# Optimization experiments

Measured on AMD Instinct MI355X. Metric: run time of the kernel, lower is better.

Reference implementation:

```python
import jax, jax.numpy as jnp
import numpy as np

EMBED_DIM = 2048
NUM_HEADS = 32
NUM_KV_HEADS = 8
HEAD_DIM = EMBED_DIM // NUM_HEADS          # 64
GROUP = NUM_HEADS // NUM_KV_HEADS          # 4 queries per KV head
BATCH, SEQ = 2, 2048


def setup_inputs() -> dict:
    key = jax.random.key(0)
    ks = jax.random.split(key, 9)
    s_in = 1.0 / np.sqrt(EMBED_DIM)
    kv_dim = NUM_KV_HEADS * HEAD_DIM
    return {
        "x":      jax.random.normal(ks[0], (BATCH, SEQ, EMBED_DIM), jnp.float32),
        "Wq":     jax.random.normal(ks[1], (EMBED_DIM, EMBED_DIM), jnp.float32) * s_in,
        "bq":     jnp.zeros((EMBED_DIM,), jnp.float32),
        "Wk":     jax.random.normal(ks[2], (EMBED_DIM, kv_dim), jnp.float32) * s_in,
        "bk":     jnp.zeros((kv_dim,), jnp.float32),
        "Wv":     jax.random.normal(ks[3], (EMBED_DIM, kv_dim), jnp.float32) * s_in,
        "bv":     jnp.zeros((kv_dim,), jnp.float32),
        "Wo":     jax.random.normal(ks[4], (EMBED_DIM, EMBED_DIM), jnp.float32) * s_in,
        "bo":     jnp.zeros((EMBED_DIM,), jnp.float32),
    }


def reference(x, Wq, bq, Wk, bk, Wv, bv, Wo, bo):
    B, S, _ = x.shape
    # Projections (torch Linear == x @ W + b with W stored as [in, out] here)
    q = (x @ Wq + bq).reshape(B, S, NUM_KV_HEADS, GROUP, HEAD_DIM)  # grouped heads
    k = (x @ Wk + bk).reshape(B, S, NUM_KV_HEADS, HEAD_DIM)
    v = (x @ Wv + bv).reshape(B, S, NUM_KV_HEADS, HEAD_DIM)

    scale = 1.0 / np.sqrt(HEAD_DIM)
    # scores[b, h, g, s, t] = q[b, s, h, g, :] . k[b, t, h, :]
    # (repeat_interleave of K across the group dim == broadcasting over g)
    scores = jnp.einsum("bshgd,bthd->bhgst", q, k) * scale
    attn = jax.nn.softmax(scores, axis=-1)
    out = jnp.einsum("bhgst,bthd->bshgd", attn, v)  # [B, S, kvh, g, D]
    out = out.reshape(B, S, EMBED_DIM)
    return out @ Wo + bo
```

## Files before the change

### kernel.cpp

```cpp
#include <hip/hip_runtime.h>


typedef __attribute__((ext_vector_type(8)))  short bf16x8;
typedef __attribute__((ext_vector_type(4)))  float f32x4;
typedef __attribute__((ext_vector_type(16))) float f32x16;

#define DEVI static __device__ __forceinline__

DEVI short f2b(float f){
  unsigned u = __builtin_bit_cast(unsigned, f);
  u += 0x7FFFu + ((u >> 16) & 1u);
  return (short)(u >> 16);
}
DEVI float b2f(short s){
  unsigned u = ((unsigned)(unsigned short)s) << 16;
  return __builtin_bit_cast(float, u);
}
DEVI unsigned pack2(float a, float b){
  unsigned ua = __builtin_bit_cast(unsigned, a) + 0x8000u;
  unsigned ub = __builtin_bit_cast(unsigned, b) + 0x8000u;
  return __builtin_amdgcn_perm(ub, ua, 0x07060302u);
}

typedef __attribute__((address_space(3))) unsigned       lds_u32;
typedef __attribute__((address_space(1))) const unsigned gbl_u32;
DEVI void glds16(const short* g, short* l){
  __builtin_amdgcn_global_load_lds((gbl_u32*)g, (lds_u32*)l, 16, 0, 0);
}

__global__ void cast_kernel(const float* __restrict__ in, short* __restrict__ out, int n){
  int i = (blockIdx.x * 256 + threadIdx.x) * 8;
  if(i >= n) return;
  float4 a = *(const float4*)(in + i);
  float4 b = *(const float4*)(in + i + 4);
  bf16x8 v;
  v[0]=f2b(a.x); v[1]=f2b(a.y); v[2]=f2b(a.z); v[3]=f2b(a.w);
  v[4]=f2b(b.x); v[5]=f2b(b.y); v[6]=f2b(b.z); v[7]=f2b(b.w);
  *(bf16x8*)(out + i) = v;
}

__global__ void prep_kernel(const float* __restrict__ Wq, const float* __restrict__ Wk,
                            const float* __restrict__ Wv, const float* __restrict__ Wo,
                            const float* __restrict__ bq, const float* __restrict__ bk,
                            const float* __restrict__ bv,
                            short* __restrict__ WT, short* __restrict__ WoT,
                            float* __restrict__ bqkv){
  __shared__ __align__(16) short tile[64*72];
  const int gy = blockIdx.y;
  const int t = threadIdx.x;
  if(gy >= 80){
    int i = blockIdx.x * 256 + t;
    if(i < 3072) bqkv[i] = (i < 2048) ? bq[i] : (i < 2560 ? bk[i-2048] : bv[i-2560]);
    return;
  }
  const float* src; short* dst; int ldin, by;
  if(gy < 32)      { src = Wq; dst = WT;             ldin = 2048; by = gy;    }
  else if(gy < 40) { src = Wk; dst = WT + 2048*2048; ldin =  512; by = gy-32; }
  else if(gy < 48) { src = Wv; dst = WT + 2560*2048; ldin =  512; by = gy-40; }
  else             { src = Wo; dst = WoT;            ldin = 2048; by = gy-48; }
  const int tr = blockIdx.x * 64;
  const int tc = by * 64;
  for(int c = t; c < 512; c += 256){
    int r = c >> 3, g = c & 7;
    const float* p = src + (size_t)(tr + r) * ldin + tc + g*8;
    bf16x8 v;
    #pragma unroll
    for(int e = 0; e < 8; e++) v[e] = f2b(p[e]);
    *(bf16x8*)&tile[r*72 + g*8] = v;
  }
  __syncthreads();
  for(int c = t; c < 512; c += 256){
    int r = c >> 3, g = c & 7;
    bf16x8 v;
    #pragma unroll
    for(int e = 0; e < 8; e++) v[e] = tile[(g*8+e)*72 + r];
    *(bf16x8*)(dst + (size_t)(tc + r) * 2048 + tr + g*8) = v;
  }
}

__global__ void transpose_bf16_kernel(const short* __restrict__ in, short* __restrict__ out,
                                      int ldin, int ldout){
  __shared__ __align__(16) short tile[64*72];
  const int tr = blockIdx.x * 64;
  const int tc = blockIdx.y * 64;
  const int t = threadIdx.x;
  for(int c = t; c < 512; c += 256){
    int r = c >> 3, g = c & 7;
    *(bf16x8*)&tile[r*72 + g*8] = *(const bf16x8*)(in + (size_t)(tr + r) * ldin + tc + g*8);
  }
  __syncthreads();
  for(int c = t; c < 512; c += 256){
    int r = c >> 3, g = c & 7;
    bf16x8 v;
    #pragma unroll
    for(int e = 0; e < 8; e++) v[e] = tile[(g*8+e)*72 + r];
    *(bf16x8*)(out + (size_t)(tc + r) * ldout + tr + g*8) = v;
  }
}

template<bool OUT_F32>
__global__ __launch_bounds__(256, 2)
void gemm_bt_kernel(const short* __restrict__ A, const short* __restrict__ BT,
                    const float* __restrict__ bias, void* __restrict__ C,
                    int M, int N, int K, int scale_cols, float qscale){
  __shared__ __align__(16) short As[128*32];
  __shared__ __align__(16) short Bs[128*32];
  const int m0 = blockIdx.x * 128;
  const int n0 = blockIdx.y * 128;
  const int tid = threadIdx.x;
  const int wave = tid >> 6, lane = tid & 63;
  const int l16 = lane & 15, quad = lane >> 4;
  const int wm = (wave >> 1) * 64, wn = (wave & 1) * 64;

  const short* gA = A  + (size_t)(m0 + wave*32 + (lane>>2))*K + (lane&3)*8;
  const short* gB = BT + (size_t)(n0 + wave*32 + (lane>>2))*K + (lane&3)*8;
  short* lA = As + wave*32*32;
  short* lB = Bs + wave*32*32;

  f32x4 acc[4][4];
  #pragma unroll
  for(int i=0;i<4;i++)
    #pragma unroll
    for(int j=0;j<4;j++) acc[i][j] = (f32x4)(0.0f);

  for(int k0 = 0; k0 < K; k0 += 32){
    glds16(gA + k0,                lA);
    glds16(gA + 16*(size_t)K + k0, lA + 512);
    glds16(gB + k0,                lB);
    glds16(gB + 16*(size_t)K + k0, lB + 512);
    __syncthreads();
    bf16x8 af[4], bfr[4];
    #pragma unroll
    for(int i=0;i<4;i++){
      af[i]  = *(const bf16x8*)&As[(wm + i*16 + l16)*32 + quad*8];
      bfr[i] = *(const bf16x8*)&Bs[(wn + i*16 + l16)*32 + quad*8];
    }
    #pragma unroll
    for(int i=0;i<4;i++)
      #pragma unroll
      for(int j=0;j<4;j++)
        acc[i][j] = __builtin_amdgcn_mfma_f32_16x16x32_bf16(af[i], bfr[j], acc[i][j], 0, 0, 0);
    __syncthreads();
  }

  #pragma unroll
  for(int j=0;j<4;j++){
    int col = n0 + wn + j*16 + l16;
    float bb = bias[col];
    float sc = (col < scale_cols) ? qscale : 1.0f;
    #pragma unroll
    for(int i=0;i<4;i++){
      #pragma unroll
      for(int r=0;r<4;r++){
        size_t row = (size_t)(m0 + wm + i*16 + quad*4 + r);
        float v = (acc[i][j][r] + bb) * sc;
        if(OUT_F32) ((float*)C)[row*(size_t)N + col] = v;
        else        ((short*)C)[row*(size_t)N + col] = f2b(v);
      }
    }
  }
}

__global__ __launch_bounds__(256, 4)
void attn_kernel(const short* __restrict__ Qg, const short* __restrict__ Kg,
                 const short* __restrict__ VT, short* __restrict__ Og, int ldq){
  const int qt  = blockIdx.x;
  const int kvh = blockIdx.y;
  const int b   = blockIdx.z;
  const int tid = threadIdx.x;
  const int wave = tid >> 6, lane = tid & 63;
  const int c = lane & 31, h = lane >> 5;
  const int head = kvh*4 + wave;
  const int q0 = qt * 32;

  __shared__ __align__(16) short Ks[64*72];
  __shared__ __align__(16) short Vs[64*72];
  __shared__ __align__(16) short Ps[4][32*72];
  __shared__ __align__(16) float lS[4][32];

  bf16x8 qreg[4];
  #pragma unroll
  for(int ks=0; ks<4; ks++)
    qreg[ks] = *(const bf16x8*)(Qg + (size_t)(b*2048 + q0 + c)*ldq + head*64 + ks*16 + h*8);

  float lsum = 0.0f;
  f32x16 oacc[2];
  oacc[0] = (f32x16)(0.0f);
  oacc[1] = (f32x16)(0.0f);

  const short* gK = Kg + (size_t)(b*2048 + (tid>>3))*ldq + kvh*64 + (tid&7)*8;
  const short* gV = VT + (size_t)(kvh*64 + (tid>>3))*4096 + b*2048 + (tid&7)*8;
  short* sK = &Ks[(tid>>3)*72 + (tid&7)*8];
  short* sV = &Vs[(tid>>3)*72 + (tid&7)*8];
  const size_t kHalf = (size_t)32 * ldq;

  bf16x8 kr0 = *(const bf16x8*)(gK);
  bf16x8 kr1 = *(const bf16x8*)(gK + kHalf);
  bf16x8 vr0 = *(const bf16x8*)(gV);
  bf16x8 vr1 = *(const bf16x8*)(gV + 32*4096);

  for(int t0 = 0; t0 < 2048; t0 += 64){
    if(t0) __syncthreads();
    *(bf16x8*)sK            = kr0;
    *(bf16x8*)(sK + 32*72)  = kr1;
    *(bf16x8*)sV            = vr0;
    *(bf16x8*)(sV + 32*72)  = vr1;
    __syncthreads();
    if(t0 + 64 < 2048){
      const short* nK = gK + (size_t)(t0 + 64)*ldq;
      const short* nV = gV + (t0 + 64);
      kr0 = *(const bf16x8*)(nK);
      kr1 = *(const bf16x8*)(nK + kHalf);
      vr0 = *(const bf16x8*)(nV);
      vr1 = *(const bf16x8*)(nV + 32*4096);
    }

    f32x16 st[2];
    st[0] = (f32x16)(0.0f);
    st[1] = (f32x16)(0.0f);
    #pragma unroll
    for(int ks=0; ks<4; ks++){
      #pragma unroll
      for(int kb=0; kb<2; kb++){
        bf16x8 ak = *(const bf16x8*)&Ks[(kb*32 + c)*72 + ks*16 + h*8];
        st[kb] = __builtin_amdgcn_mfma_f32_32x32x16_bf16(ak, qreg[ks], st[kb], 0, 0, 0);
      }
    }

    float sum = 0.0f;
    #pragma unroll
    for(int kb=0; kb<2; kb++){
      #pragma unroll
      for(int g2=0; g2<4; g2++){
        float p0 = exp2f(st[kb][g2*4+0]);
        float p1 = exp2f(st[kb][g2*4+1]);
        float p2 = exp2f(st[kb][g2*4+2]);
        float p3 = exp2f(st[kb][g2*4+3]);
        sum += (p0 + p1) + (p2 + p3);
        uint2 w; w.x = pack2(p0, p1); w.y = pack2(p2, p3);
        *(uint2*)&Ps[wave][c*72 + kb*32 + g2*8 + 4*h] = w;
      }
    }
    lsum += sum;

    #pragma unroll
    for(int ks=0; ks<4; ks++){
      bf16x8 ap = *(const bf16x8*)&Ps[wave][c*72 + ks*16 + h*8];
      #pragma unroll
      for(int nb=0; nb<2; nb++){
        bf16x8 av = *(const bf16x8*)&Vs[(nb*32 + c)*72 + ks*16 + h*8];
        oacc[nb] = __builtin_amdgcn_mfma_f32_32x32x16_bf16(ap, av, oacc[nb], 0, 0, 0);
      }
    }
  }

  lsum += __shfl_xor(lsum, 32);
  if(h == 0) lS[wave][c] = lsum;
  f32x4 l4[4];
  #pragma unroll
  for(int g2=0; g2<4; g2++){
    f32x4 t = *(const f32x4*)&lS[wave][8*g2 + 4*h];
    l4[g2][0]=1.0f/t[0]; l4[g2][1]=1.0f/t[1]; l4[g2][2]=1.0f/t[2]; l4[g2][3]=1.0f/t[3];
  }
  #pragma unroll
  for(int nb=0; nb<2; nb++){
    int col = head*64 + nb*32 + c;
    #pragma unroll
    for(int e=0; e<16; e++){
      int row = q0 + (e&3) + 8*(e>>2) + 4*h;
      Og[(size_t)(b*2048 + row)*2048 + col] = f2b(oacc[nb][e] * l4[e>>2][e&3]);
    }
  }
}

extern "C" void kernel_launch(void* const* d_in, const int* in_sizes, int n_in,
                              void* d_out, int out_size, void* d_ws, size_t ws_size,
                              hipStream_t stream){
  const float* x  = (const float*)d_in[0];
  const float* Wq = (const float*)d_in[1];
  const float* bq = (const float*)d_in[2];
  const float* Wk = (const float*)d_in[3];
  const float* bk = (const float*)d_in[4];
  const float* Wv = (const float*)d_in[5];
  const float* bv = (const float*)d_in[6];
  const float* Wo = (const float*)d_in[7];
  const float* bo = (const float*)d_in[8];

  char* ws = (char*)d_ws;
  short* WT   = (short*)(ws);
  short* WoT  = (short*)(ws + 25165824);
  short* xb   = (short*)(ws + 33554432);
  short* QKV  = (short*)(ws + 50331648);
  short* VTb  = (short*)(ws + 75497472);
  float* bqkv = (float*)(ws + 79691776);
  short* AO   = xb;

  cast_kernel<<<4096, 256, 0, stream>>>(x, xb, 8388608);
  prep_kernel<<<dim3(32,81), 256, 0, stream>>>(Wq, Wk, Wv, Wo, bq, bk, bv, WT, WoT, bqkv);

  gemm_bt_kernel<false><<<dim3(32,24), 256, 0, stream>>>(xb, WT, bqkv, QKV,
                                                         4096, 3072, 2048,
                                                         2048, 0.1803368801111244f);

  transpose_bf16_kernel<<<dim3(64,8), 256, 0, stream>>>(QKV + 2560, VTb, 3072, 4096);

  attn_kernel<<<dim3(64,8,2), 256, 0, stream>>>(QKV, QKV + 2048, VTb, AO, 3072);

  gemm_bt_kernel<true><<<dim3(32,16), 256, 0, stream>>>(AO, WoT, bo, (float*)d_out,
                                                        4096, 2048, 2048, 0, 1.0f);
}
```

Measured before the change: 346.5 us.

## Process 64 queries per attention block to reuse K/V tiles across two query groups

Each wave of the attention kernel now handles two 32-row query groups against each staged K/V tile, doubling the query tile to 64 and halving the grid. This halves global K/V loads and LDS staging per query and gives each wave more independent MFMAs to interleave. The exponential switches to the hardware exp2 builtin. The costs are more accumulator registers (launch bounds lowered to 2 blocks per SM), a larger LDS P buffer, and only 1024 blocks, which may reduce occupancy and latency hiding.

```diff
diff --git a/kernel.cpp b/kernel.cpp
--- a/kernel.cpp
+++ b/kernel.cpp
@@ -6,15 +6,17 @@
 typedef __attribute__((ext_vector_type(16))) float f32x16;
 
 #define DEVI static __device__ __forceinline__
+
+#if __has_builtin(__builtin_amdgcn_exp2f)
+#define EXP2F __builtin_amdgcn_exp2f
+#else
+#define EXP2F exp2f
+#endif
 
 DEVI short f2b(float f){
   unsigned u = __builtin_bit_cast(unsigned, f);
   u += 0x7FFFu + ((u >> 16) & 1u);
   return (short)(u >> 16);
-}
-DEVI float b2f(short s){
-  unsigned u = ((unsigned)(unsigned short)s) << 16;
-  return __builtin_bit_cast(float, u);
 }
 DEVI unsigned pack2(float a, float b){
   unsigned ua = __builtin_bit_cast(unsigned, a) + 0x8000u;
@@ -161,7 +163,7 @@
   }
 }
 
-__global__ __launch_bounds__(256, 4)
+__global__ __launch_bounds__(256, 2)
 void attn_kernel(const short* __restrict__ Qg, const short* __restrict__ Kg,
                  const short* __restrict__ VT, short* __restrict__ Og, int ldq){
   const int qt  = blockIdx.x;
@@ -171,22 +173,27 @@
   const int wave = tid >> 6, lane = tid & 63;
   const int c = lane & 31, h = lane >> 5;
   const int head = kvh*4 + wave;
-  const int q0 = qt * 32;
+  const int q0 = qt * 64;
 
   __shared__ __align__(16) short Ks[64*72];
   __shared__ __align__(16) short Vs[64*72];
-  __shared__ __align__(16) short Ps[4][32*72];
-  __shared__ __align__(16) float lS[4][32];
-
-  bf16x8 qreg[4];
+  __shared__ __align__(16) short Ps[4][64*72];
+  __shared__ __align__(16) float lS[4][2][32];
+
+  bf16x8 qreg[4][2];
   #pragma unroll
   for(int ks=0; ks<4; ks++)
-    qreg[ks] = *(const bf16x8*)(Qg + (size_t)(b*2048 + q0 + c)*ldq + head*64 + ks*16 + h*8);
-
-  float lsum = 0.0f;
-  f32x16 oacc[2];
-  oacc[0] = (f32x16)(0.0f);
-  oacc[1] = (f32x16)(0.0f);
+    #pragma unroll
+    for(int qg=0; qg<2; qg++)
+      qreg[ks][qg] = *(const bf16x8*)(Qg + (size_t)(b*2048 + q0 + qg*32 + c)*ldq
+                                         + head*64 + ks*16 + h*8);
+
+  float lsum[2] = {0.0f, 0.0f};
+  f32x16 oacc[2][2];
+  #pragma unroll
+  for(int qg=0; qg<2; qg++)
+    #pragma unroll
+    for(int nb=0; nb<2; nb++) oacc[qg][nb] = (f32x16)(0.0f);
 
   const short* gK = Kg + (size_t)(b*2048 + (tid>>3))*ldq + kvh*64 + (tid&7)*8;
   const short* gV = VT + (size_t)(kvh*64 + (tid>>3))*4096 + b*2048 + (tid&7)*8;
@@ -215,60 +222,73 @@
       vr1 = *(const bf16x8*)(nV + 32*4096);
     }
 
-    f32x16 st[2];
-    st[0] = (f32x16)(0.0f);
-    st[1] = (f32x16)(0.0f);
+    f32x16 st[2][2];
+    st[0][0] = (f32x16)(0.0f); st[0][1] = (f32x16)(0.0f);
+    st[1][0] = (f32x16)(0.0f); st[1][1] = (f32x16)(0.0f);
     #pragma unroll
     for(int ks=0; ks<4; ks++){
       #pragma unroll
       for(int kb=0; kb<2; kb++){
         bf16x8 ak = *(const bf16x8*)&Ks[(kb*32 + c)*72 + ks*16 + h*8];
-        st[kb] = __builtin_amdgcn_mfma_f32_32x32x16_bf16(ak, qreg[ks], st[kb], 0, 0, 0);
-      }
-    }
-
-    float sum = 0.0f;
-    #pragma unroll
-    for(int kb=0; kb<2; kb++){
-      #pragma unroll
-      for(int g2=0; g2<4; g2++){
-        float p0 = exp2f(st[kb][g2*4+0]);
-        float p1 = exp2f(st[kb][g2*4+1]);
-        float p2 = exp2f(st[kb][g2*4+2]);
-        float p3 = exp2f(st[kb][g2*4+3]);
-        sum += (p0 + p1) + (p2 + p3);
-        uint2 w; w.x = pack2(p0, p1); w.y = pack2(p2, p3);
-        *(uint2*)&Ps[wave][c*72 + kb*32 + g2*8 + 4*h] = w;
-      }
-    }
-    lsum += sum;
+        st[kb][0] = __builtin_amdgcn_mfma_f32_32x32x16_bf16(ak, qreg[ks][0], st[kb][0], 0, 0, 0);
+        st[kb][1] = __builtin_amdgcn_mfma_f32_32x32x16_bf16(ak, qreg[ks][1], st[kb][1], 0, 0, 0);
+      }
+    }
+
+    #pragma unroll
+    for(int qg=0; qg<2; qg++){
+      float sum = 0.0f;
+      #pragma unroll
+      for(int kb=0; kb<2; kb++){
+        #pragma unroll
+        for(int g2=0; g2<4; g2++){
+          float p0 = EXP2F(st[kb][qg][g2*4+0]);
+          float p1 = EXP2F(st[kb][qg][g2*4+1]);
+          float p2 = EXP2F(st[kb][qg][g2*4+2]);
+          float p3 = EXP2F(st[kb][qg][g2*4+3]);
+          sum += (p0 + p1) + (p2 + p3);
+          uint2 w; w.x = pack2(p0, p1); w.y = pack2(p2, p3);
+          *(uint2*)&Ps[wave][(qg*32 + c)*72 + kb*32 + g2*8 + 4*h] = w;
+        }
+      }
+      lsum[qg] += sum;
+    }
 
     #pragma unroll
     for(int ks=0; ks<4; ks++){
-      bf16x8 ap = *(const bf16x8*)&Ps[wave][c*72 + ks*16 + h*8];
+      bf16x8 ap0 = *(const bf16x8*)&Ps[wave][(c     )*72 + ks*16 + h*8];
+      bf16x8 ap1 = *(const bf16x8*)&Ps[wave][(32 + c)*72 + ks*16 + h*8];
       #pragma unroll
       for(int nb=0; nb<2; nb++){
         bf16x8 av = *(const bf16x8*)&Vs[(nb*32 + c)*72 + ks*16 + h*8];
-        oacc[nb] = __builtin_amdgcn_mfma_f32_32x32x16_bf16(ap, av, oacc[nb], 0, 0, 0);
-      }
-    }
-  }
-
-  lsum += __shfl_xor(lsum, 32);
-  if(h == 0) lS[wave][c] = lsum;
-  f32x4 l4[4];
-  #pragma unroll
-  for(int g2=0; g2<4; g2++){
-    f32x4 t = *(const f32x4*)&lS[wave][8*g2 + 4*h];
-    l4[g2][0]=1.0f/t[0]; l4[g2][1]=1.0f/t[1]; l4[g2][2]=1.0f/t[2]; l4[g2][3]=1.0f/t[3];
-  }
-  #pragma unroll
-  for(int nb=0; nb<2; nb++){
-    int col = head*64 + nb*32 + c;
-    #pragma unroll
-    for(int e=0; e<16; e++){
-      int row = q0 + (e&3) + 8*(e>>2) + 4*h;
-      Og[(size_t)(b*2048 + row)*2048 + col] = f2b(oacc[nb][e] * l4[e>>2][e&3]);
+        oacc[0][nb] = __builtin_amdgcn_mfma_f32_32x32x16_bf16(ap0, av, oacc[0][nb], 0, 0, 0);
+        oacc[1][nb] = __builtin_amdgcn_mfma_f32_32x32x16_bf16(ap1, av, oacc[1][nb], 0, 0, 0);
+      }
+    }
+  }
+
+  #pragma unroll
+  for(int qg=0; qg<2; qg++){
+    lsum[qg] += __shfl_xor(lsum[qg], 32);
+    if(h == 0) lS[wave][qg][c] = lsum[qg];
+  }
+  __builtin_amdgcn_s_waitcnt(0);
+  #pragma unroll
+  for(int qg=0; qg<2; qg++){
+    f32x4 l4[4];
+    #pragma unroll
+    for(int g2=0; g2<4; g2++){
+      f32x4 t = *(const f32x4*)&lS[wave][qg][8*g2 + 4*h];
+      l4[g2][0]=1.0f/t[0]; l4[g2][1]=1.0f/t[1]; l4[g2][2]=1.0f/t[2]; l4[g2][3]=1.0f/t[3];
+    }
+    #pragma unroll
+    for(int nb=0; nb<2; nb++){
+      int col = head*64 + nb*32 + c;
+      #pragma unroll
+      for(int e=0; e<16; e++){
+        int row = q0 + qg*32 + (e&3) + 8*(e>>2) + 4*h;
+        Og[(size_t)(b*2048 + row)*2048 + col] = f2b(oacc[qg][e>>4==0?nb:nb][e] * l4[e>>2][e&3]);
+      }
     }
   }
 }
@@ -304,7 +324,7 @@
 
   transpose_bf16_kernel<<<dim3(64,8), 256, 0, stream>>>(QKV + 2560, VTb, 3072, 4096);
 
-  attn_kernel<<<dim3(64,8,2), 256, 0, stream>>>(QKV, QKV + 2048, VTb, AO, 3072);
+  attn_kernel<<<dim3(32,8,2), 256, 0, stream>>>(QKV, QKV + 2048, VTb, AO, 3072);
 
   gemm_bt_kernel<true><<<dim3(32,16), 256, 0, stream>>>(AO, WoT, bo, (float*)d_out,
                                                         4096, 2048, 2048, 0, 1.0f);
```

Result: faster. 312.6 us (-9.8%).
